# Kernel tuning notes

Hardware: AMD Instinct MI355X
Metric: run time of the kernel (lower is better)

## Reference

```python
import jax, jax.numpy as jnp
import numpy as np

N_ITEMS = 200_000
N_USERS = 50_000
EMB = 100
BATCH = 100
HIST_MAX = 50
LAYERS = 3
NNZ_A = 6_400_000
NNZ_H = 25_000


def setup_inputs() -> dict:
    key = jax.random.key(0)
    ks = jax.random.split(key, 12)
    return dict(
        adj_row=jax.random.randint(ks[0], (NNZ_A,), 0, N_ITEMS, dtype=jnp.int32),
        adj_col=jax.random.randint(ks[1], (NNZ_A,), 0, N_ITEMS, dtype=jnp.int32),
        adj_val=jax.random.uniform(ks[2], (NNZ_A,), dtype=jnp.float32),
        hist_row=jax.random.randint(ks[3], (NNZ_H,), 0, BATCH * HIST_MAX, dtype=jnp.int32),
        hist_col=jax.random.randint(ks[4], (NNZ_H,), 0, N_ITEMS, dtype=jnp.int32),
        hist_val=jax.random.uniform(ks[5], (NNZ_H,), dtype=jnp.float32),
        hist_len=jax.random.randint(ks[6], (BATCH,), 0, HIST_MAX, dtype=jnp.int32),
        user=jax.random.randint(ks[7], (BATCH,), 0, N_USERS, dtype=jnp.int32),
        embedding=jax.random.normal(ks[8], (N_ITEMS, EMB), dtype=jnp.float32),
        user_embedding=jax.random.normal(ks[9], (N_USERS, EMB), dtype=jnp.float32),
        gamma_k=jax.random.uniform(ks[10], (LAYERS + 1,), dtype=jnp.float32),
        W_1=jax.random.normal(ks[11], (2 * EMB, 1), dtype=jnp.float32),
    )


def spmm(row, col, val, x, n_rows):
    # COO sparse @ dense: gather rows of x by col, scale, scatter-add by row.
    return jax.ops.segment_sum(val[:, None] * x[col], row, num_segments=n_rows)


def reference(adj_row, adj_col, adj_val, hist_row, hist_col, hist_val,
              hist_len, user, embedding, user_embedding, gamma_k, W_1):
    # Multi-layer hypergraph propagation with gamma-weighted accumulation.
    item = embedding
    acc = embedding * gamma_k[0]
    for i in range(LAYERS):
        item = spmm(adj_row, adj_col, adj_val, item, N_ITEMS) * gamma_k[i + 1]
        acc = acc + item
    item_embeddings = acc  # [N_ITEMS, EMB]

    # ishist=True branch: attention-masked history aggregation.
    ue = user_embedding[user]  # [B, E]
    hist_emb = spmm(hist_row, hist_col, hist_val, item_embeddings,
                    BATCH * HIST_MAX).reshape(BATCH, HIST_MAX, EMB)
    mask = jnp.arange(HIST_MAX, dtype=hist_len.dtype)[None, :] >= hist_len[:, None]
    neg = mask.astype(item_embeddings.dtype) * (-99999.0)
    # cat(query_user, hist_emb) @ W_1 == ue @ W_1[:E] + hist_emb @ W_1[E:]
    alpha = (ue @ W_1[:EMB, 0])[:, None] + jnp.einsum('bhe,e->bh', hist_emb, W_1[EMB:, 0]) + neg
    alpha = jax.nn.softmax(alpha, axis=1)  # [B, H]
    denom = jnp.where(hist_len == 0, 1, hist_len).astype(item_embeddings.dtype)
    user_out = jnp.sum(alpha[:, :, None] * hist_emb, axis=1) / denom[:, None]  # [B, E]
    return (item_embeddings, user_out)
```

## Files before the change

### kernel.cpp

```cpp
#include <hip/hip_runtime.h>
#include <hip/hip_fp16.h>

#define EMB 100
#define EMB4 25
#define SLOTS 13
#define PADH 104
#define N_ITEMS 200000
#define BATCH 100
#define HIST_MAX 50
#define ITEM_ELEMS 20000000
#define SCAN_B 1024
#define NSCAN_BLOCKS ((N_ITEMS + SCAN_B - 1) / SCAN_B)
#define VALQ 16383.0f

#define ENT 8192
#define BIN_SHIFT 10
#define ROWS_PER_BIN 1024
#define NBINS ((N_ITEMS + ROWS_PER_BIN - 1) >> BIN_SHIFT)

typedef unsigned int u32;
typedef unsigned long long u64;


__global__ void k_histogram(const int* __restrict__ row, int* __restrict__ cnt, int nnz) {
    int i = blockIdx.x * blockDim.x + threadIdx.x;
    if (i < nnz) atomicAdd(&cnt[row[i]], 1);
}

__global__ void k_scan_local(const int* __restrict__ cnt, int* __restrict__ rowptr,
                             int* __restrict__ blocksum, int n) {
    __shared__ int sd[SCAN_B];
    int b = blockIdx.x, tid = threadIdx.x;
    int i = b * SCAN_B + tid;
    int v = (i < n) ? cnt[i] : 0;
    sd[tid] = v;
    __syncthreads();
    for (int off = 1; off < SCAN_B; off <<= 1) {
        int t = (tid >= off) ? sd[tid - off] : 0;
        __syncthreads();
        sd[tid] += t;
        __syncthreads();
    }
    if (i < n) rowptr[i + 1] = sd[tid];
    if (tid == SCAN_B - 1) blocksum[b] = sd[tid];
}

__global__ void k_scan_blocks(int* __restrict__ blocksum, int nb) {
    __shared__ int sd[256];
    int tid = threadIdx.x;
    int v = (tid < nb) ? blocksum[tid] : 0;
    sd[tid] = v;
    __syncthreads();
    for (int off = 1; off < 256; off <<= 1) {
        int t = (tid >= off) ? sd[tid - off] : 0;
        __syncthreads();
        sd[tid] += t;
        __syncthreads();
    }
    if (tid < nb) blocksum[tid] = sd[tid] - v;
}

__global__ void k_scan_add(int* __restrict__ rowptr, const int* __restrict__ blocksum, int n) {
    int i = blockIdx.x * blockDim.x + threadIdx.x;
    if (i == 0) rowptr[0] = 0;
    if (i < n) rowptr[i + 1] += blocksum[i / SCAN_B];
}

__global__ __launch_bounds__(256)
void k_countbins(const int* __restrict__ row, int nnz, int nblk,
                 int* __restrict__ counts) {
    __shared__ int h[NBINS];
    int blk = blockIdx.x;
    for (int b = threadIdx.x; b < NBINS; b += 256) h[b] = 0;
    __syncthreads();
    int i0 = blk * ENT;
    int i1 = i0 + ENT; if (i1 > nnz) i1 = nnz;
    for (int i = i0 + threadIdx.x; i < i1; i += 256)
        atomicAdd(&h[row[i] >> BIN_SHIFT], 1);
    __syncthreads();
    for (int b = threadIdx.x; b < NBINS; b += 256)
        counts[b * nblk + blk] = h[b];
}

__global__ __launch_bounds__(256)
void k_binfill(const int* __restrict__ row, const int* __restrict__ col,
               const float* __restrict__ val, const int* __restrict__ offs,
               int nnz, int nblk, u64* __restrict__ stage) {
    __shared__ int base[NBINS];
    __shared__ int h[NBINS];
    int blk = blockIdx.x;
    for (int b = threadIdx.x; b < NBINS; b += 256) {
        base[b] = offs[b * nblk + blk];
        h[b] = 0;
    }
    __syncthreads();
    int i0 = blk * ENT;
    int i1 = i0 + ENT; if (i1 > nnz) i1 = nnz;
    for (int i = i0 + threadIdx.x; i < i1; i += 256) {
        int r = row[i];
        int b = r >> BIN_SHIFT;
        int rank = atomicAdd(&h[b], 1);
        u32 q = (u32)__float2uint_rn(val[i] * VALQ);
        u32 cv = ((u32)col[i] << 14) | q;
        stage[base[b] + rank] = ((u64)(u32)(r & (ROWS_PER_BIN - 1)) << 32) | cv;
    }
}

__global__ __launch_bounds__(512)
void k_place2(const u64* __restrict__ stage, const int* __restrict__ rowptr,
              u32* __restrict__ cvp) {
    __shared__ int cur[ROWS_PER_BIN];
    int b = blockIdx.x;
    int r0 = b << BIN_SHIFT;
    int rend = r0 + ROWS_PER_BIN; if (rend > N_ITEMS) rend = N_ITEMS;
    int nr = rend - r0;
    for (int i = threadIdx.x; i < nr; i += 512) cur[i] = rowptr[r0 + i];
    __syncthreads();
    int jb = rowptr[r0], je = rowptr[rend];
    for (int j = jb + threadIdx.x; j < je; j += 512) {
        u64 e = stage[j];
        int rl = (int)(e >> 32);
        int pos = atomicAdd(&cur[rl], 1);
        cvp[pos] = (u32)e;
    }
}

__global__ void k_to_half(const float* __restrict__ src, __half* __restrict__ dst) {
    int t = blockIdx.x * blockDim.x + threadIdx.x;
    if (t >= N_ITEMS * SLOTS) return;
    int r = t / SLOTS;
    int sl = t - r * SLOTS;
    int e0 = sl * 8;
    const float* s = src + r * EMB;
    __half h[8];
#pragma unroll
    for (int k = 0; k < 8; k++) {
        int e = e0 + k;
        h[k] = __float2half((e < EMB) ? s[e] : 0.f);
    }
    *(uint4*)(dst + r * PADH + e0) = *(const uint4*)h;
}


__device__ __forceinline__ void fma8(float s[8], const uint4& hv, float f) {
    const __half2* hp = reinterpret_cast<const __half2*>(&hv);
#pragma unroll
    for (int k = 0; k < 4; k++) {
        float2 p = __half22float2(hp[k]);
        s[2 * k]     += f * p.x;
        s[2 * k + 1] += f * p.y;
    }
}

__global__ void k_spmm_gather_h(const int* __restrict__ rowptr, const u32* __restrict__ cvp,
                                const __half* __restrict__ x,
                                const float* __restrict__ gamma, int gidx,
                                __half* __restrict__ outh,
                                const float* __restrict__ emb,
                                const __half* __restrict__ h1, const __half* __restrict__ h2,
                                float* __restrict__ acc) {
    int t = blockIdx.x * blockDim.x + threadIdx.x;
    if (t >= N_ITEMS * SLOTS) return;
    int r = t / SLOTS;
    int sl = t - r * SLOTS;
    int e0 = sl * 8;
    int j0 = rowptr[r], j1 = rowptr[r + 1];
    const float inv = 1.0f / VALQ;
    float s[8] = {0.f, 0.f, 0.f, 0.f, 0.f, 0.f, 0.f, 0.f};
    int j = j0;
    for (; j + 4 <= j1; j += 4) {
        u32 w0 = cvp[j + 0];
        u32 w1 = cvp[j + 1];
        u32 w2 = cvp[j + 2];
        u32 w3 = cvp[j + 3];
        uint4 v0 = *(const uint4*)(x + (w0 >> 14) * PADH + e0);
        uint4 v1 = *(const uint4*)(x + (w1 >> 14) * PADH + e0);
        uint4 v2 = *(const uint4*)(x + (w2 >> 14) * PADH + e0);
        uint4 v3 = *(const uint4*)(x + (w3 >> 14) * PADH + e0);
        fma8(s, v0, (float)(w0 & 16383u) * inv);
        fma8(s, v1, (float)(w1 & 16383u) * inv);
        fma8(s, v2, (float)(w2 & 16383u) * inv);
        fma8(s, v3, (float)(w3 & 16383u) * inv);
    }
    for (; j < j1; ++j) {
        u32 w = cvp[j];
        uint4 v = *(const uint4*)(x + (w >> 14) * PADH + e0);
        fma8(s, v, (float)(w & 16383u) * inv);
    }
    float g = gamma[gidx];
#pragma unroll
    for (int k = 0; k < 8; k++) s[k] *= g;

    if (acc) {
        float g0 = gamma[0];
        uint4 a = *(const uint4*)(h1 + r * PADH + e0);
        uint4 b = *(const uint4*)(h2 + r * PADH + e0);
        const __half2* ap = reinterpret_cast<const __half2*>(&a);
        const __half2* bp = reinterpret_cast<const __half2*>(&b);
        float o[8];
#pragma unroll
        for (int k = 0; k < 4; k++) {
            float2 pa = __half22float2(ap[k]);
            float2 pb = __half22float2(bp[k]);
            o[2 * k]     = s[2 * k]     + pa.x + pb.x;
            o[2 * k + 1] = s[2 * k + 1] + pa.y + pb.y;
        }
        const float* ep = emb + r * EMB + e0;
        float* op = acc + r * EMB + e0;
        float4 e1v = *(const float4*)(ep);
        float4 w1v = make_float4(o[0] + g0 * e1v.x, o[1] + g0 * e1v.y,
                                 o[2] + g0 * e1v.z, o[3] + g0 * e1v.w);
        *(float4*)(op) = w1v;
        if (e0 + 8 <= EMB) {
            float4 e2v = *(const float4*)(ep + 4);
            float4 w2v = make_float4(o[4] + g0 * e2v.x, o[5] + g0 * e2v.y,
                                     o[6] + g0 * e2v.z, o[7] + g0 * e2v.w);
            *(float4*)(op + 4) = w2v;
        }
    } else {
        __half hh[8];
#pragma unroll
        for (int k = 0; k < 8; k++) hh[k] = __float2half(s[k]);
        *(uint4*)(outh + r * PADH + e0) = *(const uint4*)hh;
    }
}


__global__ void k_init_acc(const float* __restrict__ emb,
                           const float* __restrict__ gamma,
                           float* __restrict__ acc, int n4) {
    int t = blockIdx.x * blockDim.x + threadIdx.x;
    if (t >= n4) return;
    float g = gamma[0];
    float4 v = ((const float4*)emb)[t];
    v.x *= g; v.y *= g; v.z *= g; v.w *= g;
    ((float4*)acc)[t] = v;
}

__global__ void k_acc_add(float* __restrict__ acc,
                          const float* __restrict__ item, int n4) {
    int t = blockIdx.x * blockDim.x + threadIdx.x;
    if (t >= n4) return;
    float4 a = ((float4*)acc)[t];
    float4 b = ((const float4*)item)[t];
    a.x += b.x; a.y += b.y; a.z += b.z; a.w += b.w;
    ((float4*)acc)[t] = a;
}

__global__ void k_spmm_atomic(const int* __restrict__ row,
                              const int* __restrict__ col,
                              const float* __restrict__ val,
                              const float* __restrict__ gamma, int gidx,
                              const float* __restrict__ x,
                              float* __restrict__ out, int nnz) {
    long long t = (long long)blockIdx.x * blockDim.x + threadIdx.x;
    long long total = (long long)nnz * EMB4;
    if (t >= total) return;
    int n = (int)(t / EMB4);
    int q = (int)(t % EMB4);
    int r = row[n];
    int c = col[n];
    float s = (gidx >= 0) ? gamma[gidx] : 1.0f;
    float v = val[n] * s;
    float4 xv = ((const float4*)x)[c * EMB4 + q];
    float* o = out + (long long)r * EMB + q * 4;
    atomicAdd(o + 0, v * xv.x);
    atomicAdd(o + 1, v * xv.y);
    atomicAdd(o + 2, v * xv.z);
    atomicAdd(o + 3, v * xv.w);
}

__global__ void k_attn(const float* __restrict__ hist_emb,
                       const int* __restrict__ hist_len,
                       const int* __restrict__ user,
                       const float* __restrict__ user_emb,
                       const float* __restrict__ W1,
                       float* __restrict__ out_user) {
    __shared__ float w[2 * EMB];
    __shared__ float he[HIST_MAX * EMB];
    __shared__ float alpha[HIST_MAX];
    __shared__ float ued, mx, sm;
    int b = blockIdx.x;
    int tid = threadIdx.x;

    for (int i = tid; i < 2 * EMB; i += blockDim.x) w[i] = W1[i];
    for (int i = tid; i < HIST_MAX * EMB; i += blockDim.x)
        he[i] = hist_emb[(long long)b * HIST_MAX * EMB + i];
    __syncthreads();

    if (tid == 0) {
        const float* ue = user_emb + (long long)user[b] * EMB;
        float s = 0.f;
        for (int e = 0; e < EMB; e++) s += ue[e] * w[e];
        ued = s;
    }
    __syncthreads();

    int len = hist_len[b];
    if (tid < HIST_MAX) {
        float d = 0.f;
        for (int e = 0; e < EMB; e++) d += he[tid * EMB + e] * w[EMB + e];
        alpha[tid] = ued + d + (tid >= len ? -99999.0f : 0.0f);
    }
    __syncthreads();

    if (tid == 0) {
        float m = -1e30f;
        for (int h = 0; h < HIST_MAX; h++) m = fmaxf(m, alpha[h]);
        mx = m;
    }
    __syncthreads();
    if (tid < HIST_MAX) alpha[tid] = expf(alpha[tid] - mx);
    __syncthreads();
    if (tid == 0) {
        float s = 0.f;
        for (int h = 0; h < HIST_MAX; h++) s += alpha[h];
        sm = s;
    }
    __syncthreads();

    float denom = (len == 0) ? 1.0f : (float)len;
    if (tid < EMB) {
        float s = 0.f;
        for (int h = 0; h < HIST_MAX; h++) s += alpha[h] * he[h * EMB + tid];
        out_user[(long long)b * EMB + tid] = s / (sm * denom);
    }
}

extern "C" void kernel_launch(void* const* d_in, const int* in_sizes, int n_in,
                              void* d_out, int out_size, void* d_ws, size_t ws_size,
                              hipStream_t stream) {
    const int*   adj_row  = (const int*)d_in[0];
    const int*   adj_col  = (const int*)d_in[1];
    const float* adj_val  = (const float*)d_in[2];
    const int*   hist_row = (const int*)d_in[3];
    const int*   hist_col = (const int*)d_in[4];
    const float* hist_val = (const float*)d_in[5];
    const int*   hist_len = (const int*)d_in[6];
    const int*   user     = (const int*)d_in[7];
    const float* embedding      = (const float*)d_in[8];
    const float* user_embedding = (const float*)d_in[9];
    const float* gamma    = (const float*)d_in[10];
    const float* W1       = (const float*)d_in[11];

    float* acc      = (float*)d_out;
    float* user_out = acc + ITEM_ELEMS;

    int nnzA = in_sizes[0];
    int nnzH = in_sizes[3];

    int nblk = (nnzA + ENT - 1) / ENT;
    int countsN = NBINS * nblk;
    int nsb = (countsN + SCAN_B - 1) / SCAN_B;

    const size_t HBT = (size_t)N_ITEMS * PADH * sizeof(__half);
    char* ws = (char*)d_ws;
    __half* hb0 = (__half*)(ws + 0 * HBT);
    __half* hb1 = (__half*)(ws + 1 * HBT);
    __half* hb2 = (__half*)(ws + 2 * HBT);
    u64*    stage = (u64*)(ws + 1 * HBT);
    float*  buf1 = (float*)(ws + 0);
    float*  buf2 = (float*)(ws + 80000000ULL);
    size_t off = 3 * HBT;
    u32*   cvp  = (u32*)(ws + off);       off += (size_t)nnzA * 4;
    int*   rowptr = (int*)(ws + off);     off += ((size_t)N_ITEMS + 4) * 4;
    int*   cnt  = (int*)(ws + off);       off += (size_t)N_ITEMS * 4;
    int*   blocksum = (int*)(ws + off);   off += 256 * 4;
    int*   blocksum2 = (int*)(ws + off);  off += 256 * 4;
    int*   counts = (int*)(ws + off);     off += (size_t)countsN * 4;
    int*   offs = (int*)(ws + off);       off += ((size_t)countsN + 8) * 4;
    float* histe = (float*)(ws + off);    off += (size_t)BATCH * HIST_MAX * EMB * 4;
    size_t need_csr = off;
    if ((size_t)nnzA * 8 > 2 * HBT) need_csr = (size_t)1 << 62;
    if (nsb > 256) need_csr = (size_t)1 << 62;

    const int n4 = ITEM_ELEMS / 4;
    long long totH = (long long)nnzH * EMB4;
    int blocksH = (int)((totH + 255) / 256);

    if (ws_size >= need_csr) {
        hipMemsetAsync(cnt, 0, (size_t)N_ITEMS * 4, stream);
        hipMemsetAsync(histe, 0, (size_t)BATCH * HIST_MAX * EMB * 4, stream);

        int bN = (nnzA + 255) / 256;
        k_histogram<<<bN, 256, 0, stream>>>(adj_row, cnt, nnzA);
        k_scan_local<<<NSCAN_BLOCKS, SCAN_B, 0, stream>>>(cnt, rowptr, blocksum, N_ITEMS);
        k_scan_blocks<<<1, 256, 0, stream>>>(blocksum, NSCAN_BLOCKS);
        k_scan_add<<<(N_ITEMS + 255) / 256, 256, 0, stream>>>(rowptr, blocksum, N_ITEMS);
        k_countbins<<<nblk, 256, 0, stream>>>(adj_row, nnzA, nblk, counts);
        k_scan_local<<<nsb, SCAN_B, 0, stream>>>(counts, offs, blocksum2, countsN);
        k_scan_blocks<<<1, 256, 0, stream>>>(blocksum2, nsb);
        k_scan_add<<<(countsN + 255) / 256, 256, 0, stream>>>(offs, blocksum2, countsN);
        k_binfill<<<nblk, 256, 0, stream>>>(adj_row, adj_col, adj_val, offs, nnzA, nblk, stage);
        k_place2<<<NBINS, 512, 0, stream>>>(stage, rowptr, cvp);

        int gThreads = N_ITEMS * SLOTS;
        int gBlocks = (gThreads + 255) / 256;
        k_to_half<<<gBlocks, 256, 0, stream>>>(embedding, hb0);
        k_spmm_gather_h<<<gBlocks, 256, 0, stream>>>(rowptr, cvp, hb0, gamma, 1,
                                                     hb1, nullptr, nullptr, nullptr, nullptr);
        k_spmm_gather_h<<<gBlocks, 256, 0, stream>>>(rowptr, cvp, hb1, gamma, 2,
                                                     hb2, nullptr, nullptr, nullptr, nullptr);
        k_spmm_gather_h<<<gBlocks, 256, 0, stream>>>(rowptr, cvp, hb2, gamma, 3,
                                                     nullptr, embedding, hb1, hb2, acc);
    } else {
        hipMemsetAsync(buf1, 0, 80000000ULL, stream);
        hipMemsetAsync(buf2, 0, 80000000ULL, stream);
        hipMemsetAsync(histe, 0, (size_t)BATCH * HIST_MAX * EMB * 4, stream);

        k_init_acc<<<(n4 + 255) / 256, 256, 0, stream>>>(embedding, gamma, acc, n4);
        long long totA = (long long)nnzA * EMB4;
        int blocksA = (int)((totA + 255) / 256);
        k_spmm_atomic<<<blocksA, 256, 0, stream>>>(adj_row, adj_col, adj_val, gamma, 1,
                                                   embedding, buf1, nnzA);
        k_acc_add<<<(n4 + 255) / 256, 256, 0, stream>>>(acc, buf1, n4);
        k_spmm_atomic<<<blocksA, 256, 0, stream>>>(adj_row, adj_col, adj_val, gamma, 2,
                                                   buf1, buf2, nnzA);
        k_acc_add<<<(n4 + 255) / 256, 256, 0, stream>>>(acc, buf2, n4);
        k_spmm_atomic<<<blocksA, 256, 0, stream>>>(adj_row, adj_col, adj_val, gamma, 3,
                                                   buf2, acc, nnzA);
    }

    k_spmm_atomic<<<blocksH, 256, 0, stream>>>(hist_row, hist_col, hist_val, gamma, -1,
                                               acc, histe, nnzH);

    k_attn<<<BATCH, 128, 0, stream>>>(histe, hist_len, user, user_embedding, W1, user_out);
}
```

Baseline: 1.584 ms.

## Fuse CSR preprocessing kernels and use half embedding in final accumulate

```diff
diff --git a/kernel.cpp b/kernel.cpp
--- a/kernel.cpp
+++ b/kernel.cpp
@@ -21,18 +21,54 @@
 typedef unsigned int u32;
 typedef unsigned long long u64;
 
-
-__global__ void k_histogram(const int* __restrict__ row, int* __restrict__ cnt, int nnz) {
-    int i = blockIdx.x * blockDim.x + threadIdx.x;
-    if (i < nnz) atomicAdd(&cnt[row[i]], 1);
-}
-
-__global__ void k_scan_local(const int* __restrict__ cnt, int* __restrict__ rowptr,
-                             int* __restrict__ blocksum, int n) {
+__global__ __launch_bounds__(256)
+void k_prep(const int* __restrict__ row, int nnz, int nblk,
+            int* __restrict__ cnt, int* __restrict__ counts,
+            const float* __restrict__ emb_src, __half* __restrict__ hb0) {
+    int blk = blockIdx.x;
+    if (blk < nblk) {
+        __shared__ int h[NBINS];
+        for (int b = threadIdx.x; b < NBINS; b += 256) h[b] = 0;
+        __syncthreads();
+        int i0 = blk * ENT;
+        int i1 = i0 + ENT; if (i1 > nnz) i1 = nnz;
+        for (int i = i0 + threadIdx.x; i < i1; i += 256) {
+            int r = row[i];
+            atomicAdd(&cnt[r], 1);
+            atomicAdd(&h[r >> BIN_SHIFT], 1);
+        }
+        __syncthreads();
+        for (int b = threadIdx.x; b < NBINS; b += 256)
+            counts[b * nblk + blk] = h[b];
+    } else {
+        int t = (blk - nblk) * 256 + threadIdx.x;
+        if (t >= N_ITEMS * SLOTS) return;
+        int r = t / SLOTS;
+        int sl = t - r * SLOTS;
+        int e0 = sl * 8;
+        const float* s = emb_src + r * EMB;
+        __half hh[8];
+#pragma unroll
+        for (int k = 0; k < 8; k++) {
+            int e = e0 + k;
+            hh[k] = __float2half((e < EMB) ? s[e] : 0.f);
+        }
+        *(uint4*)(hb0 + r * PADH + e0) = *(const uint4*)hh;
+    }
+}
+
+
+__global__ void k_scan_dual(const int* __restrict__ a, int* __restrict__ outa,
+                            int* __restrict__ bsuma, int na, int nba,
+                            const int* __restrict__ b, int* __restrict__ outb,
+                            int* __restrict__ bsumb, int nb) {
     __shared__ int sd[SCAN_B];
-    int b = blockIdx.x, tid = threadIdx.x;
-    int i = b * SCAN_B + tid;
-    int v = (i < n) ? cnt[i] : 0;
+    int blk = blockIdx.x, tid = threadIdx.x;
+    const int* src; int* out; int* bsum; int n; int lb;
+    if (blk < nba) { src = a; out = outa; bsum = bsuma; n = na; lb = blk; }
+    else           { src = b; out = outb; bsum = bsumb; n = nb; lb = blk - nba; }
+    int i = lb * SCAN_B + tid;
+    int v = (i < n) ? src[i] : 0;
     sd[tid] = v;
     __syncthreads();
     for (int off = 1; off < SCAN_B; off <<= 1) {
@@ -41,14 +77,15 @@
         sd[tid] += t;
         __syncthreads();
     }
-    if (i < n) rowptr[i + 1] = sd[tid];
-    if (tid == SCAN_B - 1) blocksum[b] = sd[tid];
-}
-
-__global__ void k_scan_blocks(int* __restrict__ blocksum, int nb) {
+    if (i < n) out[i + 1] = sd[tid];
+    if (tid == SCAN_B - 1) bsum[lb] = sd[tid];
+}
+
+__global__ void k_scan_blocks_dual(int* __restrict__ ba, int nba,
+                                   int* __restrict__ bb, int nbb) {
     __shared__ int sd[256];
     int tid = threadIdx.x;
-    int v = (tid < nb) ? blocksum[tid] : 0;
+    int v = (tid < nba) ? ba[tid] : 0;
     sd[tid] = v;
     __syncthreads();
     for (int off = 1; off < 256; off <<= 1) {
@@ -57,29 +94,34 @@
         sd[tid] += t;
         __syncthreads();
     }
-    if (tid < nb) blocksum[tid] = sd[tid] - v;
-}
-
-__global__ void k_scan_add(int* __restrict__ rowptr, const int* __restrict__ blocksum, int n) {
-    int i = blockIdx.x * blockDim.x + threadIdx.x;
-    if (i == 0) rowptr[0] = 0;
-    if (i < n) rowptr[i + 1] += blocksum[i / SCAN_B];
-}
-
-__global__ __launch_bounds__(256)
-void k_countbins(const int* __restrict__ row, int nnz, int nblk,
-                 int* __restrict__ counts) {
-    __shared__ int h[NBINS];
+    if (tid < nba) ba[tid] = sd[tid] - v;
+    __syncthreads();
+    v = (tid < nbb) ? bb[tid] : 0;
+    sd[tid] = v;
+    __syncthreads();
+    for (int off = 1; off < 256; off <<= 1) {
+        int t = (tid >= off) ? sd[tid - off] : 0;
+        __syncthreads();
+        sd[tid] += t;
+        __syncthreads();
+    }
+    if (tid < nbb) bb[tid] = sd[tid] - v;
+}
+
+__global__ void k_scan_add_dual(int* __restrict__ outa, const int* __restrict__ ba,
+                                int na, int nblka,
+                                int* __restrict__ outb, const int* __restrict__ bb,
+                                int nb) {
     int blk = blockIdx.x;
-    for (int b = threadIdx.x; b < NBINS; b += 256) h[b] = 0;
-    __syncthreads();
-    int i0 = blk * ENT;
-    int i1 = i0 + ENT; if (i1 > nnz) i1 = nnz;
-    for (int i = i0 + threadIdx.x; i < i1; i += 256)
-        atomicAdd(&h[row[i] >> BIN_SHIFT], 1);
-    __syncthreads();
-    for (int b = threadIdx.x; b < NBINS; b += 256)
-        counts[b * nblk + blk] = h[b];
+    if (blk < nblka) {
+        int i = blk * 256 + threadIdx.x;
+        if (i == 0) outa[0] = 0;
+        if (i < na) outa[i + 1] += ba[i / SCAN_B];
+    } else {
+        int i = (blk - nblka) * 256 + threadIdx.x;
+        if (i == 0) outb[0] = 0;
+        if (i < nb) outb[i + 1] += bb[i / SCAN_B];
+    }
 }
 
 __global__ __launch_bounds__(256)
@@ -125,22 +167,6 @@
     }
 }
 
-__global__ void k_to_half(const float* __restrict__ src, __half* __restrict__ dst) {
-    int t = blockIdx.x * blockDim.x + threadIdx.x;
-    if (t >= N_ITEMS * SLOTS) return;
-    int r = t / SLOTS;
-    int sl = t - r * SLOTS;
-    int e0 = sl * 8;
-    const float* s = src + r * EMB;
-    __half h[8];
-#pragma unroll
-    for (int k = 0; k < 8; k++) {
-        int e = e0 + k;
-        h[k] = __float2half((e < EMB) ? s[e] : 0.f);
-    }
-    *(uint4*)(dst + r * PADH + e0) = *(const uint4*)h;
-}
-
 
 __device__ __forceinline__ void fma8(float s[8], const uint4& hv, float f) {
     const __half2* hp = reinterpret_cast<const __half2*>(&hv);
@@ -156,7 +182,7 @@
                                 const __half* __restrict__ x,
                                 const float* __restrict__ gamma, int gidx,
                                 __half* __restrict__ outh,
-                                const float* __restrict__ emb,
+                                const __half* __restrict__ embh,
                                 const __half* __restrict__ h1, const __half* __restrict__ h2,
                                 float* __restrict__ acc) {
     int t = blockIdx.x * blockDim.x + threadIdx.x;
@@ -195,28 +221,23 @@
         float g0 = gamma[0];
         uint4 a = *(const uint4*)(h1 + r * PADH + e0);
         uint4 b = *(const uint4*)(h2 + r * PADH + e0);
+        uint4 e = *(const uint4*)(embh + r * PADH + e0);
         const __half2* ap = reinterpret_cast<const __half2*>(&a);
         const __half2* bp = reinterpret_cast<const __half2*>(&b);
+        const __half2* ep = reinterpret_cast<const __half2*>(&e);
         float o[8];
 #pragma unroll
         for (int k = 0; k < 4; k++) {
             float2 pa = __half22float2(ap[k]);
             float2 pb = __half22float2(bp[k]);
-            o[2 * k]     = s[2 * k]     + pa.x + pb.x;
-            o[2 * k + 1] = s[2 * k + 1] + pa.y + pb.y;
+            float2 pe = __half22float2(ep[k]);
+            o[2 * k]     = s[2 * k]     + pa.x + pb.x + g0 * pe.x;
+            o[2 * k + 1] = s[2 * k + 1] + pa.y + pb.y + g0 * pe.y;
         }
-        const float* ep = emb + r * EMB + e0;
         float* op = acc + r * EMB + e0;
-        float4 e1v = *(const float4*)(ep);
-        float4 w1v = make_float4(o[0] + g0 * e1v.x, o[1] + g0 * e1v.y,
-                                 o[2] + g0 * e1v.z, o[3] + g0 * e1v.w);
-        *(float4*)(op) = w1v;
-        if (e0 + 8 <= EMB) {
-            float4 e2v = *(const float4*)(ep + 4);
-            float4 w2v = make_float4(o[4] + g0 * e2v.x, o[5] + g0 * e2v.y,
-                                     o[6] + g0 * e2v.z, o[7] + g0 * e2v.w);
-            *(float4*)(op + 4) = w2v;
-        }
+        *(float4*)(op) = make_float4(o[0], o[1], o[2], o[3]);
+        if (e0 + 8 <= EMB)
+            *(float4*)(op + 4) = make_float4(o[4], o[5], o[6], o[7]);
     } else {
         __half hh[8];
 #pragma unroll
@@ -382,27 +403,28 @@
         hipMemsetAsync(cnt, 0, (size_t)N_ITEMS * 4, stream);
         hipMemsetAsync(histe, 0, (size_t)BATCH * HIST_MAX * EMB * 4, stream);
 
-        int bN = (nnzA + 255) / 256;
-        k_histogram<<<bN, 256, 0, stream>>>(adj_row, cnt, nnzA);
-        k_scan_local<<<NSCAN_BLOCKS, SCAN_B, 0, stream>>>(cnt, rowptr, blocksum, N_ITEMS);
-        k_scan_blocks<<<1, 256, 0, stream>>>(blocksum, NSCAN_BLOCKS);
-        k_scan_add<<<(N_ITEMS + 255) / 256, 256, 0, stream>>>(rowptr, blocksum, N_ITEMS);
-        k_countbins<<<nblk, 256, 0, stream>>>(adj_row, nnzA, nblk, counts);
-        k_scan_local<<<nsb, SCAN_B, 0, stream>>>(counts, offs, blocksum2, countsN);
-        k_scan_blocks<<<1, 256, 0, stream>>>(blocksum2, nsb);
-        k_scan_add<<<(countsN + 255) / 256, 256, 0, stream>>>(offs, blocksum2, countsN);
+        int gThreads = N_ITEMS * SLOTS;
+        int gBlocks = (gThreads + 255) / 256;
+
+        k_prep<<<nblk + gBlocks, 256, 0, stream>>>(adj_row, nnzA, nblk,
+                                                   cnt, counts, embedding, hb0);
+        k_scan_dual<<<NSCAN_BLOCKS + nsb, SCAN_B, 0, stream>>>(
+            cnt, rowptr, blocksum, N_ITEMS, NSCAN_BLOCKS,
+            counts, offs, blocksum2, countsN);
+        k_scan_blocks_dual<<<1, 256, 0, stream>>>(blocksum, NSCAN_BLOCKS, blocksum2, nsb);
+        int nba = (N_ITEMS + 255) / 256;
+        int nbb = (countsN + 255) / 256;
+        k_scan_add_dual<<<nba + nbb, 256, 0, stream>>>(rowptr, blocksum, N_ITEMS, nba,
+                                                       offs, blocksum2, countsN);
         k_binfill<<<nblk, 256, 0, stream>>>(adj_row, adj_col, adj_val, offs, nnzA, nblk, stage);
         k_place2<<<NBINS, 512, 0, stream>>>(stage, rowptr, cvp);
 
-        int gThreads = N_ITEMS * SLOTS;
-        int gBlocks = (gThreads + 255) / 256;
-        k_to_half<<<gBlocks, 256, 0, stream>>>(embedding, hb0);
         k_spmm_gather_h<<<gBlocks, 256, 0, stream>>>(rowptr, cvp, hb0, gamma, 1,
                                                      hb1, nullptr, nullptr, nullptr, nullptr);
         k_spmm_gather_h<<<gBlocks, 256, 0, stream>>>(rowptr, cvp, hb1, gamma, 2,
                                                      hb2, nullptr, nullptr, nullptr, nullptr);
         k_spmm_gather_h<<<gBlocks, 256, 0, stream>>>(rowptr, cvp, hb2, gamma, 3,
-                                                     nullptr, embedding, hb1, hb2, acc);
+                                                     nullptr, hb0, hb1, hb2, acc);
     } else {
         hipMemsetAsync(buf1, 0, 80000000ULL, stream);
         hipMemsetAsync(buf2, 0, 80000000ULL, stream);
```

Result: faster. 1.542 ms (-2.6%).
